# Optimization experiments

Hardware: AMD Instinct MI355X
Metric: run time of the kernel (lower is better)

The kernel has to match this reference:

```python
import jax, jax.numpy as jnp
import numpy as np

F = 128
NRBF = 20
CUTOFF = 5.0
L = 3
NZ = 100
F2 = F // 2
N = 10000
E = 256000
NMOL = 100
EPS = 1e-8


def setup_inputs() -> dict:
    key = jax.random.key(0)
    ks = jax.random.split(key, 20)
    xyz = jax.random.uniform(ks[0], (N, 3), jnp.float32) * 10.0
    z = jax.random.randint(ks[1], (N,), 0, NZ)
    nbrs = jax.random.randint(ks[2], (E, 2), 0, N)
    # avoid self-edges (would give zero distance in the sinc RBF)
    nbrs = nbrs.at[:, 1].set(jnp.where(nbrs[:, 1] == nbrs[:, 0], (nbrs[:, 1] + 1) % N, nbrs[:, 1]))
    mol_idx = jnp.sort(jax.random.randint(ks[3], (N,), 0, NMOL))

    def p(k, shape, scale=0.05):
        return jax.random.normal(k, shape, jnp.float32) * scale

    return dict(
        xyz=xyz, z=z, nbrs=nbrs, mol_idx=mol_idx,
        emb=p(ks[4], (NZ, F), 1.0),
        msg_W1=p(ks[5], (L, F, F)), msg_b1=jnp.zeros((L, F), jnp.float32),
        msg_W2=p(ks[6], (L, F, 3 * F)), msg_b2=jnp.zeros((L, 3 * F), jnp.float32),
        dist_W=p(ks[7], (L, NRBF, 3 * F)), dist_b=jnp.zeros((L, 3 * F), jnp.float32),
        upd_U=p(ks[8], (L, F, F)), upd_V=p(ks[9], (L, F, F)),
        upd_W1=p(ks[10], (L, 2 * F, F)), upd_b1=jnp.zeros((L, F), jnp.float32),
        upd_W2=p(ks[11], (L, F, 3 * F)), upd_b2=jnp.zeros((L, 3 * F), jnp.float32),
        read_W1=p(ks[12], (F, F2)), read_b1=jnp.zeros((F2,), jnp.float32),
        read_W2=p(ks[13], (F2, 1)), read_b2=jnp.zeros((1,), jnp.float32),
    )


def _painn(xyz, emb, msg_W1, msg_b1, msg_W2, msg_b2, dist_W, dist_b,
           upd_U, upd_V, upd_W1, upd_b1, upd_W2, upd_b2,
           read_W1, read_b1, read_W2, read_b2, z, nbrs, mol_idx):
    idx_i = nbrs[:, 0]
    idx_j = nbrs[:, 1]
    r_ij = xyz[idx_j] - xyz[idx_i]                       # [E,3]
    d = jnp.sqrt(jnp.sum(r_ij * r_ij, -1) + EPS)          # [E]
    unit = r_ij / d[:, None]
    # sinc radial basis + cosine cutoff envelope
    nvec = jnp.arange(1, NRBF + 1, dtype=xyz.dtype)
    rbf = jnp.sin(nvec[None, :] * jnp.pi * d[:, None] / CUTOFF) / d[:, None]   # [E,NRBF]
    fcut = 0.5 * (jnp.cos(jnp.pi * d / CUTOFF) + 1.0) * (d < CUTOFF)           # [E]

    s_i = emb[z]                                          # [N,F]
    v_i = jnp.zeros((xyz.shape[0], F, 3), xyz.dtype)      # [N,F,3]

    for l in range(L):
        # message block: invariant filter on nodes, gather to edges
        phi = (jax.nn.silu(s_i @ msg_W1[l] + msg_b1[l]) @ msg_W2[l] + msg_b2[l])[idx_j]  # [E,3F]
        w_s = (rbf @ dist_W[l] + dist_b[l]) * fcut[:, None]                               # [E,3F]
        inv = (phi * w_s).reshape(-1, 3, F)
        ds_edge = inv[:, 0]                                                               # [E,F]
        dv_edge = inv[:, 1][:, :, None] * v_i[idx_j] + inv[:, 2][:, :, None] * unit[:, None, :]  # [E,F,3]
        s_i = s_i + jax.ops.segment_sum(ds_edge, idx_i, num_segments=s_i.shape[0])
        v_i = v_i + jax.ops.segment_sum(dv_edge, idx_i, num_segments=s_i.shape[0])

        # update block: channel-mixing of vectors + gated scalar/vector residuals
        u_v = jnp.einsum('nfv,fg->ngv', v_i, upd_U[l])
        v_v = jnp.einsum('nfv,fg->ngv', v_i, upd_V[l])
        vnorm = jnp.sqrt(jnp.sum(v_v * v_v, -1) + EPS)                                    # [N,F]
        a = (jax.nn.silu(jnp.concatenate([s_i, vnorm], -1) @ upd_W1[l] + upd_b1[l])
             @ upd_W2[l] + upd_b2[l]).reshape(-1, 3, F)
        dv = u_v * a[:, 0][:, :, None]
        ds = a[:, 1] * jnp.sum(u_v * v_v, -1) + a[:, 2]
        s_i = s_i + ds
        v_i = v_i + dv

    atom_e = jax.nn.silu(s_i @ read_W1 + read_b1) @ read_W2 + read_b2                     # [N,1]
    energy = jax.ops.segment_sum(atom_e[:, 0], mol_idx, num_segments=NMOL)                # [NMOL]
    return energy


def reference(xyz, z, nbrs, mol_idx, emb, msg_W1, msg_b1, msg_W2, msg_b2,
              dist_W, dist_b, upd_U, upd_V, upd_W1, upd_b1, upd_W2, upd_b2,
              read_W1, read_b1, read_W2, read_b2):
    return _painn(xyz, emb, msg_W1, msg_b1, msg_W2, msg_b2, dist_W, dist_b,
                  upd_U, upd_V, upd_W1, upd_b1, upd_W2, upd_b2,
                  read_W1, read_b1, read_W2, read_b2, z, nbrs, mol_idx)
```

## Files before the change

### kernel.cpp

```cpp
#include <hip/hip_runtime.h>
#include <hip/hip_bf16.h>
#include <math.h>

#define NA 10000
#define NE 256000
#define FDIM 128
#define F3 384
#define NRBF 20
#define NLAYERS 3
#define NMOLS 100
#define CAP 96
#define WROW 388
#define CUTOFF_F 5.0f
#define EPS_F 1e-8f
#define PI_F 3.14159265358979323846f

typedef __attribute__((ext_vector_type(8))) short bf16x8;
typedef __attribute__((ext_vector_type(4))) short bf16x4;
typedef __attribute__((ext_vector_type(4))) float f32x4;

__device__ __forceinline__ float silu_f(float x) { return x / (1.0f + __expf(-x)); }

__device__ __forceinline__ unsigned short f2bf(float x) {
  unsigned u = __float_as_uint(x);
  return (unsigned short)((u + 0x7FFFu + ((u >> 16) & 1u)) >> 16);
}
__device__ __forceinline__ float bf2f(unsigned short u) {
  return __uint_as_float(((unsigned)u) << 16);
}

__global__ __launch_bounds__(256) void geom_build_kernel(
    const float* __restrict__ xyz, const int* __restrict__ nbrs,
    float* __restrict__ unitv, unsigned short* __restrict__ rbf_bf,
    float* __restrict__ fcut,
    int* __restrict__ deg, int* __restrict__ slot_e, int* __restrict__ slot_j) {
  int e = blockIdx.x * 256 + threadIdx.x;
  if (e >= NE) return;
  int i = nbrs[2 * e + 0], j = nbrs[2 * e + 1];
  float rx = xyz[3 * j + 0] - xyz[3 * i + 0];
  float ry = xyz[3 * j + 1] - xyz[3 * i + 1];
  float rz = xyz[3 * j + 2] - xyz[3 * i + 2];
  float d = sqrtf(rx * rx + ry * ry + rz * rz + EPS_F);
  if (d >= CUTOFF_F) return;
  float invd = 1.0f / d;
  float fc = 0.5f * (__cosf(PI_F * d / CUTOFF_F) + 1.0f);
  unitv[3 * e + 0] = rx * invd;
  unitv[3 * e + 1] = ry * invd;
  unitv[3 * e + 2] = rz * invd;
  fcut[e] = fc;
  float base = PI_F * d / CUTOFF_F;
  float sc = invd * fc;
#pragma unroll
  for (int k = 0; k < NRBF; k++)
    rbf_bf[(size_t)e * NRBF + k] = f2bf(__sinf((float)(k + 1) * base) * sc);
  int pos = atomicAdd(&deg[i], 1);
  if (pos < CAP) {
    slot_e[i * CAP + pos] = e;
    slot_j[i * CAP + pos] = j;
  }
}

__device__ __forceinline__ void pack_one(const float* __restrict__ src,
                                         unsigned short* __restrict__ dst,
                                         int loc, int per, int N) {
  int lay = loc / per;
  int kn = loc - lay * per;
  int k = kn / N, n = kn - k * N;
  int kb = k >> 5, q = (k >> 3) & 3, j = k & 7, nt = n >> 4, c = n & 15;
  int NT = N >> 4;
  dst[(size_t)lay * per + (((kb * NT + nt) * 64 + (q * 16 + c)) * 8 + j)] = f2bf(src[loc]);
}

__device__ __forceinline__ void pack_dw(const float* __restrict__ dW,
                                        const float* __restrict__ db,
                                        unsigned short* __restrict__ dst, int loc) {
  int lay = loc / 12288;
  int kn = loc - lay * 12288;
  int k = kn / 384, n = kn - k * 384;
  float val = 0.0f;
  if (k < NRBF) val = dW[lay * NRBF * 384 + k * 384 + n];
  else if (k == NRBF) val = db[lay * 384 + n];
  int q = (k >> 3) & 3, j = k & 7, nt = n >> 4, c = n & 15;
  dst[(size_t)lay * 12288 + ((nt * 64 + (q * 16 + c)) * 8 + j)] = f2bf(val);
}

__global__ __launch_bounds__(256) void pack_all_kernel(
    const float* __restrict__ msgW1, const float* __restrict__ msgW2,
    const float* __restrict__ updU, const float* __restrict__ updV,
    const float* __restrict__ updW1, const float* __restrict__ updW2,
    const float* __restrict__ rW1, const float* __restrict__ distW,
    const float* __restrict__ distb, unsigned short* __restrict__ dst) {
  int t = blockIdx.x * 256 + threadIdx.x;
  if (t < 49152) pack_one(msgW1, dst, t, 16384, 128);
  else if (t < 196608) pack_one(msgW2, dst + 49152, t - 49152, 49152, 384);
  else if (t < 245760) pack_one(updU, dst + 196608, t - 196608, 16384, 128);
  else if (t < 294912) pack_one(updV, dst + 245760, t - 245760, 16384, 128);
  else if (t < 393216) pack_one(updW1, dst + 294912, t - 294912, 32768, 128);
  else if (t < 540672) pack_one(updW2, dst + 393216, t - 393216, 49152, 384);
  else if (t < 548864) pack_one(rW1, dst + 540672, t - 540672, 8192, 64);
  else if (t < 585728) pack_dw(distW, distb, dst + 548864, t - 548864);
}

__global__ __launch_bounds__(256) void msg0_mfma_kernel(
    const float* __restrict__ emb, const int* __restrict__ z, float* __restrict__ s_out,
    const unsigned short* __restrict__ pW1, const float* __restrict__ b1,
    const unsigned short* __restrict__ pW2, const float* __restrict__ b2,
    bf16x4* __restrict__ phi4) {
  __shared__ bf16x8 sA[4 * 64];
  __shared__ bf16x8 hA[4 * 64];
  int a0 = blockIdx.x * 16;
  int t = threadIdx.x;
  int lane = t & 63, w = t >> 6;
  {
    int kb = t >> 6, l = t & 63;
    int m = l & 15, q = l >> 4;
    int zi = z[a0 + m];
    const float* sp = emb + (size_t)zi * FDIM + kb * 32 + q * 8;
    float* so = s_out + (size_t)(a0 + m) * FDIM + kb * 32 + q * 8;
    bf16x8 c;
#pragma unroll
    for (int j = 0; j < 8; j++) {
      float v = sp[j];
      so[j] = v;
      c[j] = (short)f2bf(v);
    }
    sA[kb * 64 + l] = c;
  }
  __syncthreads();
  f32x4 accH[2];
#pragma unroll
  for (int t2 = 0; t2 < 2; t2++)
#pragma unroll
    for (int r = 0; r < 4; r++) accH[t2][r] = 0.0f;
  const bf16x8* W1f = (const bf16x8*)pW1;
#pragma unroll
  for (int kb = 0; kb < 4; kb++) {
    bf16x8 a = sA[kb * 64 + lane];
#pragma unroll
    for (int t2 = 0; t2 < 2; t2++) {
      bf16x8 b = W1f[(kb * 8 + 2 * w + t2) * 64 + lane];
      accH[t2] = __builtin_amdgcn_mfma_f32_16x16x32_bf16(a, b, accH[t2], 0, 0, 0);
    }
  }
  short* hs = (short*)hA;
#pragma unroll
  for (int t2 = 0; t2 < 2; t2++) {
    int n = w * 32 + t2 * 16 + (lane & 15);
    int kb = n >> 5, q = (n >> 3) & 3, j = n & 7;
    float bias = b1[n];
#pragma unroll
    for (int r = 0; r < 4; r++) {
      int m = (lane >> 4) * 4 + r;
      hs[(kb * 64 + q * 16 + m) * 8 + j] = (short)f2bf(silu_f(accH[t2][r] + bias));
    }
  }
  __syncthreads();
  f32x4 accP[3][2];
#pragma unroll
  for (int c3 = 0; c3 < 3; c3++)
#pragma unroll
    for (int t2 = 0; t2 < 2; t2++)
#pragma unroll
      for (int r = 0; r < 4; r++) accP[c3][t2][r] = 0.0f;
  const bf16x8* W2f = (const bf16x8*)pW2;
#pragma unroll
  for (int kb = 0; kb < 4; kb++) {
    bf16x8 a = hA[kb * 64 + lane];
#pragma unroll
    for (int c3 = 0; c3 < 3; c3++)
#pragma unroll
      for (int t2 = 0; t2 < 2; t2++) {
        bf16x8 b = W2f[(kb * 24 + c3 * 8 + 2 * w + t2) * 64 + lane];
        accP[c3][t2] = __builtin_amdgcn_mfma_f32_16x16x32_bf16(a, b, accP[c3][t2], 0, 0, 0);
      }
  }
#pragma unroll
  for (int t2 = 0; t2 < 2; t2++) {
    int g = (2 * w + t2) * 16 + (lane & 15);
    float bb0 = b2[g], bb1 = b2[FDIM + g], bb2 = b2[2 * FDIM + g];
#pragma unroll
    for (int r = 0; r < 4; r++) {
      int m = (lane >> 4) * 4 + r;
      bf16x4 pw;
      pw[0] = (short)f2bf(accP[0][t2][r] + bb0);
      pw[1] = (short)f2bf(accP[1][t2][r] + bb1);
      pw[2] = (short)f2bf(accP[2][t2][r] + bb2);
      pw[3] = 0;
      phi4[(size_t)(a0 + m) * FDIM + g] = pw;
    }
  }
}

__global__ __launch_bounds__(128) void edge_kernel(
    const bf16x4* __restrict__ phi4, const bf16x4* __restrict__ vpad4,
    unsigned short* __restrict__ v_lin, float* __restrict__ s,
    const unsigned short* __restrict__ pDW,
    const int* __restrict__ deg, const int* __restrict__ slot_e,
    const int* __restrict__ slot_j, const unsigned short* __restrict__ rbf_bf,
    const float* __restrict__ fcut, const float* __restrict__ unitv, int vzero) {
  __shared__ bf16x8 aLDS[64];
  __shared__ unsigned short w_lds[16][WROW];
  __shared__ float l_u[16][3];
  __shared__ int l_j[16];
  int i = blockIdx.x;
  int t = threadIdx.x;
  int f = t;
  int lane = t & 63, w = t >> 6;
  int cnt = deg[i];
  if (cnt > CAP) cnt = CAP;
  int base = i * CAP;
  float acc_s = 0.f, av0 = 0.f, av1 = 0.f, av2 = 0.f;
  const bf16x8* Bf = (const bf16x8*)pDW;
  for (int c0 = 0; c0 < cnt; c0 += 16) {
    int ccnt = cnt - c0;
    if (ccnt > 16) ccnt = 16;
    __syncthreads();
    if (t < 64) {
      int m = t & 15, q = t >> 4;
      bf16x8 a;
#pragma unroll
      for (int j = 0; j < 8; j++) a[j] = 0;
      int p = c0 + m;
      if (p < cnt) {
        int e = slot_e[base + p];
        const unsigned short* rb = rbf_bf + (size_t)e * NRBF;
#pragma unroll
        for (int j = 0; j < 8; j++) {
          int k = q * 8 + j;
          if (k < NRBF) a[j] = (short)rb[k];
          else if (k == NRBF) a[j] = (short)f2bf(fcut[e]);
        }
      }
      aLDS[t] = a;
    } else if (t < 80) {
      int idx = t - 64;
      int p = c0 + idx;
      if (p < cnt) {
        int e = slot_e[base + p];
        l_j[idx] = slot_j[base + p];
        l_u[idx][0] = unitv[3 * e + 0];
        l_u[idx][1] = unitv[3 * e + 1];
        l_u[idx][2] = unitv[3 * e + 2];
      }
    }
    __syncthreads();
    {
      bf16x8 a = aLDS[lane];
      int n0 = lane & 15, m0 = (lane >> 4) * 4;
#pragma unroll
      for (int tt = 0; tt < 12; tt++) {
        int nt = 12 * w + tt;
        f32x4 acc;
#pragma unroll
        for (int r = 0; r < 4; r++) acc[r] = 0.0f;
        acc = __builtin_amdgcn_mfma_f32_16x16x32_bf16(a, Bf[nt * 64 + lane], acc, 0, 0, 0);
        int n = nt * 16 + n0;
#pragma unroll
        for (int r = 0; r < 4; r++) w_lds[m0 + r][n] = f2bf(acc[r]);
      }
    }
    __syncthreads();
    int pp = 0;
    for (; pp + 2 <= ccnt; pp += 2) {
      int j0 = l_j[pp], j1 = l_j[pp + 1];
      bf16x4 P0 = phi4[(size_t)j0 * FDIM + f];
      bf16x4 P1 = phi4[(size_t)j1 * FDIM + f];
      float v00 = 0.f, v01 = 0.f, v02 = 0.f, v10 = 0.f, v11 = 0.f, v12 = 0.f;
      if (!vzero) {
        bf16x4 V0 = vpad4[(size_t)j0 * FDIM + f];
        bf16x4 V1 = vpad4[(size_t)j1 * FDIM + f];
        v00 = bf2f((unsigned short)V0[0]); v01 = bf2f((unsigned short)V0[1]); v02 = bf2f((unsigned short)V0[2]);
        v10 = bf2f((unsigned short)V1[0]); v11 = bf2f((unsigned short)V1[1]); v12 = bf2f((unsigned short)V1[2]);
      }
      float p00 = bf2f((unsigned short)P0[0]), p01 = bf2f((unsigned short)P0[1]), p02 = bf2f((unsigned short)P0[2]);
      float p10 = bf2f((unsigned short)P1[0]), p11 = bf2f((unsigned short)P1[1]), p12 = bf2f((unsigned short)P1[2]);
      float w00 = bf2f(w_lds[pp][f]), w01 = bf2f(w_lds[pp][FDIM + f]),
            w02 = bf2f(w_lds[pp][2 * FDIM + f]);
      float w10 = bf2f(w_lds[pp + 1][f]), w11 = bf2f(w_lds[pp + 1][FDIM + f]),
            w12 = bf2f(w_lds[pp + 1][2 * FDIM + f]);
      acc_s += p00 * w00 + p10 * w10;
      float i01 = p01 * w01, i02 = p02 * w02, i11 = p11 * w11, i12 = p12 * w12;
      av0 += i01 * v00 + i02 * l_u[pp][0] + i11 * v10 + i12 * l_u[pp + 1][0];
      av1 += i01 * v01 + i02 * l_u[pp][1] + i11 * v11 + i12 * l_u[pp + 1][1];
      av2 += i01 * v02 + i02 * l_u[pp][2] + i11 * v12 + i12 * l_u[pp + 1][2];
    }
    if (pp < ccnt) {
      int j0 = l_j[pp];
      bf16x4 P0 = phi4[(size_t)j0 * FDIM + f];
      float v00 = 0.f, v01 = 0.f, v02 = 0.f;
      if (!vzero) {
        bf16x4 V0 = vpad4[(size_t)j0 * FDIM + f];
        v00 = bf2f((unsigned short)V0[0]); v01 = bf2f((unsigned short)V0[1]); v02 = bf2f((unsigned short)V0[2]);
      }
      float p00 = bf2f((unsigned short)P0[0]), p01 = bf2f((unsigned short)P0[1]), p02 = bf2f((unsigned short)P0[2]);
      float w00 = bf2f(w_lds[pp][f]), w01 = bf2f(w_lds[pp][FDIM + f]),
            w02 = bf2f(w_lds[pp][2 * FDIM + f]);
      acc_s += p00 * w00;
      float i01 = p01 * w01, i02 = p02 * w02;
      av0 += i01 * v00 + i02 * l_u[pp][0];
      av1 += i01 * v01 + i02 * l_u[pp][1];
      av2 += i01 * v02 + i02 * l_u[pp][2];
    }
  }
  if (!vzero) {
    bf16x4 VI = vpad4[(size_t)i * FDIM + f];
    av0 += bf2f((unsigned short)VI[0]);
    av1 += bf2f((unsigned short)VI[1]);
    av2 += bf2f((unsigned short)VI[2]);
  }
  unsigned short* vlo = v_lin + (size_t)i * F3;
  vlo[f] = f2bf(av0);
  vlo[FDIM + f] = f2bf(av1);
  vlo[2 * FDIM + f] = f2bf(av2);
  s[(size_t)i * FDIM + f] += acc_s;
}

__global__ __launch_bounds__(256) void upd_fused_kernel(
    float* __restrict__ s, const unsigned short* __restrict__ v_lin,
    bf16x4* __restrict__ vpad4,
    const unsigned short* __restrict__ pU, const unsigned short* __restrict__ pV,
    const unsigned short* __restrict__ pW1, const float* __restrict__ b1,
    const unsigned short* __restrict__ pW2, const float* __restrict__ b2,
    int mode,
    const unsigned short* __restrict__ pMW1, const float* __restrict__ mb1,
    const unsigned short* __restrict__ pMW2, const float* __restrict__ mb2,
    bf16x4* __restrict__ phi4,
    const unsigned short* __restrict__ pRW1, const float* __restrict__ rb1,
    const float* __restrict__ rW2, const float* __restrict__ rb2,
    float* __restrict__ atom_e) {
  __shared__ bf16x8 vAf[3 * 4 * 64];
  __shared__ bf16x8 catA[8 * 64];
  __shared__ bf16x8 hA[4 * 64];
  __shared__ float red[4][16];
  int a0 = blockIdx.x * 16;
  int t = threadIdx.x;
  int lane = t & 63, w = t >> 6;
  {
    int l = t & 63, kb = (t >> 6) & 3;
    int m = l & 15, q = l >> 4;
#pragma unroll
    for (int rt = 0; rt < 3; rt++) {
      vAf[(rt * 4 + kb) * 64 + l] =
          *(const bf16x8*)(v_lin + (size_t)(a0 + m) * F3 + rt * FDIM + kb * 32 + q * 8);
    }
    const float* sp = s + (size_t)(a0 + m) * FDIM + kb * 32 + q * 8;
    bf16x8 c;
#pragma unroll
    for (int j = 0; j < 8; j++) c[j] = (short)f2bf(sp[j]);
    catA[kb * 64 + l] = c;
  }
  __syncthreads();
  f32x4 accU[3][2], accV[3][2];
#pragma unroll
  for (int rt = 0; rt < 3; rt++)
#pragma unroll
    for (int t2 = 0; t2 < 2; t2++)
#pragma unroll
      for (int r = 0; r < 4; r++) { accU[rt][t2][r] = 0.0f; accV[rt][t2][r] = 0.0f; }
  const bf16x8* Uf = (const bf16x8*)pU;
  const bf16x8* Vf = (const bf16x8*)pV;
#pragma unroll
  for (int kb = 0; kb < 4; kb++) {
    bf16x8 bu[2], bv[2];
#pragma unroll
    for (int t2 = 0; t2 < 2; t2++) {
      bu[t2] = Uf[(kb * 8 + 2 * w + t2) * 64 + lane];
      bv[t2] = Vf[(kb * 8 + 2 * w + t2) * 64 + lane];
    }
#pragma unroll
    for (int rt = 0; rt < 3; rt++) {
      bf16x8 a = vAf[(rt * 4 + kb) * 64 + lane];
#pragma unroll
      for (int t2 = 0; t2 < 2; t2++) {
        accU[rt][t2] = __builtin_amdgcn_mfma_f32_16x16x32_bf16(a, bu[t2], accU[rt][t2], 0, 0, 0);
        accV[rt][t2] = __builtin_amdgcn_mfma_f32_16x16x32_bf16(a, bv[t2], accV[rt][t2], 0, 0, 0);
      }
    }
  }
  short* cs = (short*)catA;
#pragma unroll
  for (int t2 = 0; t2 < 2; t2++) {
    int g = w * 32 + t2 * 16 + (lane & 15);
    int k = 128 + g;
    int kb = k >> 5, q = (k >> 3) & 3, j = k & 7;
#pragma unroll
    for (int r = 0; r < 4; r++) {
      int m = (lane >> 4) * 4 + r;
      float x0 = accV[0][t2][r], x1 = accV[1][t2][r], x2 = accV[2][t2][r];
      cs[(kb * 64 + q * 16 + m) * 8 + j] = (short)f2bf(sqrtf(x0 * x0 + x1 * x1 + x2 * x2 + EPS_F));
    }
  }
  __syncthreads();
  f32x4 accH[2];
#pragma unroll
  for (int t2 = 0; t2 < 2; t2++)
#pragma unroll
    for (int r = 0; r < 4; r++) accH[t2][r] = 0.0f;
  const bf16x8* W1f = (const bf16x8*)pW1;
#pragma unroll
  for (int kb = 0; kb < 8; kb++) {
    bf16x8 a = catA[kb * 64 + lane];
#pragma unroll
    for (int t2 = 0; t2 < 2; t2++) {
      bf16x8 b = W1f[(kb * 8 + 2 * w + t2) * 64 + lane];
      accH[t2] = __builtin_amdgcn_mfma_f32_16x16x32_bf16(a, b, accH[t2], 0, 0, 0);
    }
  }
  short* hs = (short*)hA;
#pragma unroll
  for (int t2 = 0; t2 < 2; t2++) {
    int n = w * 32 + t2 * 16 + (lane & 15);
    int kb = n >> 5, q = (n >> 3) & 3, j = n & 7;
    float bias = b1[n];
#pragma unroll
    for (int r = 0; r < 4; r++) {
      int m = (lane >> 4) * 4 + r;
      hs[(kb * 64 + q * 16 + m) * 8 + j] = (short)f2bf(silu_f(accH[t2][r] + bias));
    }
  }
  __syncthreads();
  f32x4 accA[3][2];
#pragma unroll
  for (int c3 = 0; c3 < 3; c3++)
#pragma unroll
    for (int t2 = 0; t2 < 2; t2++)
#pragma unroll
      for (int r = 0; r < 4; r++) accA[c3][t2][r] = 0.0f;
  const bf16x8* W2f = (const bf16x8*)pW2;
#pragma unroll
  for (int kb = 0; kb < 4; kb++) {
    bf16x8 a = hA[kb * 64 + lane];
#pragma unroll
    for (int c3 = 0; c3 < 3; c3++)
#pragma unroll
      for (int t2 = 0; t2 < 2; t2++) {
        bf16x8 b = W2f[(kb * 24 + c3 * 8 + 2 * w + t2) * 64 + lane];
        accA[c3][t2] = __builtin_amdgcn_mfma_f32_16x16x32_bf16(a, b, accA[c3][t2], 0, 0, 0);
      }
  }
#pragma unroll
  for (int t2 = 0; t2 < 2; t2++) {
    int g = w * 32 + t2 * 16 + (lane & 15);
    float bb0 = b2[g], bb1 = b2[FDIM + g], bb2 = b2[2 * FDIM + g];
    int kb = g >> 5, q = (g >> 3) & 3, j = g & 7;
#pragma unroll
    for (int r = 0; r < 4; r++) {
      int m = (lane >> 4) * 4 + r;
      int n = a0 + m;
      float a0v = accA[0][t2][r] + bb0;
      float a1v = accA[1][t2][r] + bb1;
      float a2v = accA[2][t2][r] + bb2;
      float dot = accU[0][t2][r] * accV[0][t2][r] + accU[1][t2][r] * accV[1][t2][r] +
                  accU[2][t2][r] * accV[2][t2][r];
      float s_new = s[(size_t)n * FDIM + g] + a1v * dot + a2v;
      if (mode == 0) {
        s[(size_t)n * FDIM + g] = s_new;
        bf16x4 vw;
#pragma unroll
        for (int c = 0; c < 3; c++) {
          float nv = bf2f(v_lin[(size_t)n * F3 + c * FDIM + g]) + a0v * accU[c][t2][r];
          vw[c] = (short)f2bf(nv);
        }
        vw[3] = 0;
        vpad4[(size_t)n * FDIM + g] = vw;
      }
      cs[(kb * 64 + q * 16 + m) * 8 + j] = (short)f2bf(s_new);
    }
  }
  __syncthreads();
  if (mode == 0) {
    f32x4 accH2[2];
#pragma unroll
    for (int t2 = 0; t2 < 2; t2++)
#pragma unroll
      for (int r = 0; r < 4; r++) accH2[t2][r] = 0.0f;
    const bf16x8* MW1f = (const bf16x8*)pMW1;
#pragma unroll
    for (int kb = 0; kb < 4; kb++) {
      bf16x8 a = catA[kb * 64 + lane];
#pragma unroll
      for (int t2 = 0; t2 < 2; t2++) {
        bf16x8 b = MW1f[(kb * 8 + 2 * w + t2) * 64 + lane];
        accH2[t2] = __builtin_amdgcn_mfma_f32_16x16x32_bf16(a, b, accH2[t2], 0, 0, 0);
      }
    }
#pragma unroll
    for (int t2 = 0; t2 < 2; t2++) {
      int n = w * 32 + t2 * 16 + (lane & 15);
      int kb = n >> 5, q = (n >> 3) & 3, j = n & 7;
      float bias = mb1[n];
#pragma unroll
      for (int r = 0; r < 4; r++) {
        int m = (lane >> 4) * 4 + r;
        hs[(kb * 64 + q * 16 + m) * 8 + j] = (short)f2bf(silu_f(accH2[t2][r] + bias));
      }
    }
    __syncthreads();
    f32x4 accP[3][2];
#pragma unroll
    for (int c3 = 0; c3 < 3; c3++)
#pragma unroll
      for (int t2 = 0; t2 < 2; t2++)
#pragma unroll
        for (int r = 0; r < 4; r++) accP[c3][t2][r] = 0.0f;
    const bf16x8* MW2f = (const bf16x8*)pMW2;
#pragma unroll
    for (int kb = 0; kb < 4; kb++) {
      bf16x8 a = hA[kb * 64 + lane];
#pragma unroll
      for (int c3 = 0; c3 < 3; c3++)
#pragma unroll
        for (int t2 = 0; t2 < 2; t2++) {
          bf16x8 b = MW2f[(kb * 24 + c3 * 8 + 2 * w + t2) * 64 + lane];
          accP[c3][t2] = __builtin_amdgcn_mfma_f32_16x16x32_bf16(a, b, accP[c3][t2], 0, 0, 0);
        }
    }
#pragma unroll
    for (int t2 = 0; t2 < 2; t2++) {
      int g = (2 * w + t2) * 16 + (lane & 15);
      float bb0 = mb2[g], bb1 = mb2[FDIM + g], bb2v = mb2[2 * FDIM + g];
#pragma unroll
      for (int r = 0; r < 4; r++) {
        int m = (lane >> 4) * 4 + r;
        bf16x4 pw;
        pw[0] = (short)f2bf(accP[0][t2][r] + bb0);
        pw[1] = (short)f2bf(accP[1][t2][r] + bb1);
        pw[2] = (short)f2bf(accP[2][t2][r] + bb2v);
        pw[3] = 0;
        phi4[(size_t)(a0 + m) * FDIM + g] = pw;
      }
    }
  } else {
    f32x4 acc;
#pragma unroll
    for (int r = 0; r < 4; r++) acc[r] = 0.0f;
    const bf16x8* RW1f = (const bf16x8*)pRW1;
#pragma unroll
    for (int kb = 0; kb < 4; kb++) {
      bf16x8 a = catA[kb * 64 + lane];
      bf16x8 b = RW1f[(kb * 4 + w) * 64 + lane];
      acc = __builtin_amdgcn_mfma_f32_16x16x32_bf16(a, b, acc, 0, 0, 0);
    }
    int col = w * 16 + (lane & 15);
    float bias = rb1[col], w2v = rW2[col];
    float val[4];
#pragma unroll
    for (int r = 0; r < 4; r++) val[r] = silu_f(acc[r] + bias) * w2v;
#pragma unroll
    for (int off = 1; off < 16; off <<= 1)
#pragma unroll
      for (int r = 0; r < 4; r++) val[r] += __shfl_xor(val[r], off, 64);
    if ((lane & 15) == 0) {
#pragma unroll
      for (int r = 0; r < 4; r++) red[w][(lane >> 4) * 4 + r] = val[r];
    }
    __syncthreads();
    if (t < 16) {
      atom_e[a0 + t] = red[0][t] + red[1][t] + red[2][t] + red[3][t] + rb2[0];
    }
  }
}

__global__ __launch_bounds__(256) void mol_reduce_kernel(
    const float* __restrict__ atom_e, const int* __restrict__ mol_idx,
    float* __restrict__ out) {
  __shared__ float molsum[NMOLS];
  int t = threadIdx.x;
  if (t < NMOLS) molsum[t] = 0.0f;
  __syncthreads();
  int n = blockIdx.x * 256 + t;
  if (n < NA) atomicAdd(&molsum[mol_idx[n]], atom_e[n]);
  __syncthreads();
  if (t < NMOLS && molsum[t] != 0.0f) atomicAdd(&out[t], molsum[t]);
}

extern "C" void kernel_launch(void* const* d_in, const int* in_sizes, int n_in,
                              void* d_out, int out_size, void* d_ws, size_t ws_size,
                              hipStream_t stream) {
  const float* xyz = (const float*)d_in[0];
  const int* z = (const int*)d_in[1];
  const int* nbrs = (const int*)d_in[2];
  const int* mol = (const int*)d_in[3];
  const float* emb = (const float*)d_in[4];
  const float* msgW1 = (const float*)d_in[5];
  const float* msgb1 = (const float*)d_in[6];
  const float* msgW2 = (const float*)d_in[7];
  const float* msgb2 = (const float*)d_in[8];
  const float* distW = (const float*)d_in[9];
  const float* distb = (const float*)d_in[10];
  const float* updU = (const float*)d_in[11];
  const float* updV = (const float*)d_in[12];
  const float* updW1 = (const float*)d_in[13];
  const float* updb1 = (const float*)d_in[14];
  const float* updW2 = (const float*)d_in[15];
  const float* updb2 = (const float*)d_in[16];
  const float* rW1 = (const float*)d_in[17];
  const float* rb1 = (const float*)d_in[18];
  const float* rW2 = (const float*)d_in[19];
  const float* rb2 = (const float*)d_in[20];

  float* ws = (float*)d_ws;
  float* s = ws;      ws += (size_t)NA * FDIM;
  float* fcut = ws;   ws += (size_t)NE;
  float* unitv = ws;  ws += (size_t)NE * 3;
  float* atom_e = ws; ws += (size_t)NA;
  int* deg = (int*)ws;
  int* slot_e = deg + NA;
  int* slot_j = slot_e + NA * CAP;
  unsigned short* pk = (unsigned short*)(((uintptr_t)(slot_j + NA * CAP) + 15) & ~(uintptr_t)15);
  unsigned short* pMsgW1 = pk;
  unsigned short* pMsgW2 = pMsgW1 + 49152;
  unsigned short* pUpdU  = pMsgW2 + 147456;
  unsigned short* pUpdV  = pUpdU + 49152;
  unsigned short* pUpdW1 = pUpdV + 49152;
  unsigned short* pUpdW2 = pUpdW1 + 98304;
  unsigned short* pRW1   = pUpdW2 + 147456;
  unsigned short* pDW    = pRW1 + 8192;
  unsigned short* rbf_bf = (unsigned short*)(((uintptr_t)(pDW + 36864) + 15) & ~(uintptr_t)15);
  unsigned short* after_rbf = rbf_bf + (size_t)NE * NRBF + 8;
  bf16x4* phi4 = (bf16x4*)(((uintptr_t)after_rbf + 15) & ~(uintptr_t)15);
  bf16x4* vpad4 = phi4 + (size_t)NA * FDIM;
  unsigned short* v_lin = (unsigned short*)(vpad4 + (size_t)NA * FDIM);

  hipMemsetAsync(deg, 0, NA * sizeof(int), stream);
  hipMemsetAsync(d_out, 0, NMOLS * sizeof(float), stream);

  pack_all_kernel<<<(585728 + 255) / 256, 256, 0, stream>>>(
      msgW1, msgW2, updU, updV, updW1, updW2, rW1, distW, distb, pMsgW1);
  geom_build_kernel<<<NE / 256, 256, 0, stream>>>(xyz, nbrs, unitv, rbf_bf, fcut,
                                                  deg, slot_e, slot_j);
  msg0_mfma_kernel<<<NA / 16, 256, 0, stream>>>(emb, z, s, pMsgW1, msgb1, pMsgW2, msgb2, phi4);

  for (int l = 0; l < NLAYERS; l++) {
    edge_kernel<<<NA, 128, 0, stream>>>(phi4, vpad4, v_lin, s,
                                        pDW + (size_t)l * 12288,
                                        deg, slot_e, slot_j, rbf_bf, fcut, unitv,
                                        (l == 0) ? 1 : 0);
    int mode = (l == NLAYERS - 1) ? 1 : 0;
    int lnext = (l + 1 < NLAYERS) ? l + 1 : 0;
    upd_fused_kernel<<<NA / 16, 256, 0, stream>>>(
        s, v_lin, vpad4, pUpdU + (size_t)l * 16384, pUpdV + (size_t)l * 16384,
        pUpdW1 + (size_t)l * 32768, updb1 + (size_t)l * FDIM,
        pUpdW2 + (size_t)l * 49152, updb2 + (size_t)l * F3,
        mode,
        pMsgW1 + (size_t)lnext * 16384, msgb1 + (size_t)lnext * FDIM,
        pMsgW2 + (size_t)lnext * 49152, msgb2 + (size_t)lnext * F3,
        phi4, pRW1, rb1, rW2, rb2, atom_e);
  }
  mol_reduce_kernel<<<(NA + 255) / 256, 256, 0, stream>>>(atom_e, mol, (float*)d_out);
}
```

Before: 337.7 us.

## Interleave phi and vector features into one packed 12-byte record per atom-feature

The separate padded phi and v gather arrays are merged into a single 6-bf16 record per atom and feature. The edge kernel now issues one 12-byte gather per neighbour instead of two 8-byte gathers, which cuts gathered bytes and memory requests in the later layers. The update kernel stages the new v values in shared memory so they can be written alongside the next layer's phi. The trade-off is that layer 0 now loads the zero-filled v fields it previously skipped, and reusing the shared-memory buffer adds an aliasing risk.

After: 326.4 us. 1.03x faster.

```diff
diff --git a/kernel.cpp b/kernel.cpp
--- a/kernel.cpp
+++ b/kernel.cpp
@@ -16,8 +16,9 @@
 #define PI_F 3.14159265358979323846f
 
 typedef __attribute__((ext_vector_type(8))) short bf16x8;
-typedef __attribute__((ext_vector_type(4))) short bf16x4;
 typedef __attribute__((ext_vector_type(4))) float f32x4;
+
+struct pv6 { unsigned int u0, u1, u2; };
 
 __device__ __forceinline__ float silu_f(float x) { return x / (1.0f + __expf(-x)); }
 
@@ -28,6 +29,8 @@
 __device__ __forceinline__ float bf2f(unsigned short u) {
   return __uint_as_float(((unsigned)u) << 16);
 }
+__device__ __forceinline__ float lo_f(unsigned int u) { return bf2f((unsigned short)(u & 0xFFFFu)); }
+__device__ __forceinline__ float hi_f(unsigned int u) { return bf2f((unsigned short)(u >> 16)); }
 
 __global__ __launch_bounds__(256) void geom_build_kernel(
     const float* __restrict__ xyz, const int* __restrict__ nbrs,
@@ -105,7 +108,7 @@
     const float* __restrict__ emb, const int* __restrict__ z, float* __restrict__ s_out,
     const unsigned short* __restrict__ pW1, const float* __restrict__ b1,
     const unsigned short* __restrict__ pW2, const float* __restrict__ b2,
-    bf16x4* __restrict__ phi4) {
+    pv6* __restrict__ cmb) {
   __shared__ bf16x8 sA[4 * 64];
   __shared__ bf16x8 hA[4 * 64];
   int a0 = blockIdx.x * 16;
@@ -181,23 +184,24 @@
 #pragma unroll
     for (int r = 0; r < 4; r++) {
       int m = (lane >> 4) * 4 + r;
-      bf16x4 pw;
-      pw[0] = (short)f2bf(accP[0][t2][r] + bb0);
-      pw[1] = (short)f2bf(accP[1][t2][r] + bb1);
-      pw[2] = (short)f2bf(accP[2][t2][r] + bb2);
-      pw[3] = 0;
-      phi4[(size_t)(a0 + m) * FDIM + g] = pw;
+      unsigned p0 = f2bf(accP[0][t2][r] + bb0);
+      unsigned p1 = f2bf(accP[1][t2][r] + bb1);
+      unsigned p2 = f2bf(accP[2][t2][r] + bb2);
+      pv6 rec;
+      rec.u0 = p0 | (p1 << 16);
+      rec.u1 = p2;
+      rec.u2 = 0;
+      cmb[(size_t)(a0 + m) * FDIM + g] = rec;
     }
   }
 }
 
 __global__ __launch_bounds__(128) void edge_kernel(
-    const bf16x4* __restrict__ phi4, const bf16x4* __restrict__ vpad4,
-    unsigned short* __restrict__ v_lin, float* __restrict__ s,
-    const unsigned short* __restrict__ pDW,
+    const pv6* __restrict__ cmb, unsigned short* __restrict__ v_lin,
+    float* __restrict__ s, const unsigned short* __restrict__ pDW,
     const int* __restrict__ deg, const int* __restrict__ slot_e,
     const int* __restrict__ slot_j, const unsigned short* __restrict__ rbf_bf,
-    const float* __restrict__ fcut, const float* __restrict__ unitv, int vzero) {
+    const float* __restrict__ fcut, const float* __restrict__ unitv) {
   __shared__ bf16x8 aLDS[64];
   __shared__ unsigned short w_lds[16][WROW];
   __shared__ float l_u[16][3];
@@ -263,17 +267,12 @@
     int pp = 0;
     for (; pp + 2 <= ccnt; pp += 2) {
       int j0 = l_j[pp], j1 = l_j[pp + 1];
-      bf16x4 P0 = phi4[(size_t)j0 * FDIM + f];
-      bf16x4 P1 = phi4[(size_t)j1 * FDIM + f];
-      float v00 = 0.f, v01 = 0.f, v02 = 0.f, v10 = 0.f, v11 = 0.f, v12 = 0.f;
-      if (!vzero) {
-        bf16x4 V0 = vpad4[(size_t)j0 * FDIM + f];
-        bf16x4 V1 = vpad4[(size_t)j1 * FDIM + f];
-        v00 = bf2f((unsigned short)V0[0]); v01 = bf2f((unsigned short)V0[1]); v02 = bf2f((unsigned short)V0[2]);
-        v10 = bf2f((unsigned short)V1[0]); v11 = bf2f((unsigned short)V1[1]); v12 = bf2f((unsigned short)V1[2]);
-      }
-      float p00 = bf2f((unsigned short)P0[0]), p01 = bf2f((unsigned short)P0[1]), p02 = bf2f((unsigned short)P0[2]);
-      float p10 = bf2f((unsigned short)P1[0]), p11 = bf2f((unsigned short)P1[1]), p12 = bf2f((unsigned short)P1[2]);
+      pv6 R0 = cmb[(size_t)j0 * FDIM + f];
+      pv6 R1 = cmb[(size_t)j1 * FDIM + f];
+      float p00 = lo_f(R0.u0), p01 = hi_f(R0.u0), p02 = lo_f(R0.u1);
+      float v00 = hi_f(R0.u1), v01 = lo_f(R0.u2), v02 = hi_f(R0.u2);
+      float p10 = lo_f(R1.u0), p11 = hi_f(R1.u0), p12 = lo_f(R1.u1);
+      float v10 = hi_f(R1.u1), v11 = lo_f(R1.u2), v12 = hi_f(R1.u2);
       float w00 = bf2f(w_lds[pp][f]), w01 = bf2f(w_lds[pp][FDIM + f]),
             w02 = bf2f(w_lds[pp][2 * FDIM + f]);
       float w10 = bf2f(w_lds[pp + 1][f]), w11 = bf2f(w_lds[pp + 1][FDIM + f]),
@@ -286,13 +285,9 @@
     }
     if (pp < ccnt) {
       int j0 = l_j[pp];
-      bf16x4 P0 = phi4[(size_t)j0 * FDIM + f];
-      float v00 = 0.f, v01 = 0.f, v02 = 0.f;
-      if (!vzero) {
-        bf16x4 V0 = vpad4[(size_t)j0 * FDIM + f];
-        v00 = bf2f((unsigned short)V0[0]); v01 = bf2f((unsigned short)V0[1]); v02 = bf2f((unsigned short)V0[2]);
-      }
-      float p00 = bf2f((unsigned short)P0[0]), p01 = bf2f((unsigned short)P0[1]), p02 = bf2f((unsigned short)P0[2]);
+      pv6 R0 = cmb[(size_t)j0 * FDIM + f];
+      float p00 = lo_f(R0.u0), p01 = hi_f(R0.u0), p02 = lo_f(R0.u1);
+      float v00 = hi_f(R0.u1), v01 = lo_f(R0.u2), v02 = hi_f(R0.u2);
       float w00 = bf2f(w_lds[pp][f]), w01 = bf2f(w_lds[pp][FDIM + f]),
             w02 = bf2f(w_lds[pp][2 * FDIM + f]);
       acc_s += p00 * w00;
@@ -302,11 +297,11 @@
       av2 += i01 * v02 + i02 * l_u[pp][2];
     }
   }
-  if (!vzero) {
-    bf16x4 VI = vpad4[(size_t)i * FDIM + f];
-    av0 += bf2f((unsigned short)VI[0]);
-    av1 += bf2f((unsigned short)VI[1]);
-    av2 += bf2f((unsigned short)VI[2]);
+  {
+    pv6 RI = cmb[(size_t)i * FDIM + f];
+    av0 += hi_f(RI.u1);
+    av1 += lo_f(RI.u2);
+    av2 += hi_f(RI.u2);
   }
   unsigned short* vlo = v_lin + (size_t)i * F3;
   vlo[f] = f2bf(av0);
@@ -317,14 +312,13 @@
 
 __global__ __launch_bounds__(256) void upd_fused_kernel(
     float* __restrict__ s, const unsigned short* __restrict__ v_lin,
-    bf16x4* __restrict__ vpad4,
+    pv6* __restrict__ cmb,
     const unsigned short* __restrict__ pU, const unsigned short* __restrict__ pV,
     const unsigned short* __restrict__ pW1, const float* __restrict__ b1,
     const unsigned short* __restrict__ pW2, const float* __restrict__ b2,
     int mode,
     const unsigned short* __restrict__ pMW1, const float* __restrict__ mb1,
     const unsigned short* __restrict__ pMW2, const float* __restrict__ mb2,
-    bf16x4* __restrict__ phi4,
     const unsigned short* __restrict__ pRW1, const float* __restrict__ rb1,
     const float* __restrict__ rW2, const float* __restrict__ rb2,
     float* __restrict__ atom_e) {
@@ -438,6 +432,7 @@
         accA[c3][t2] = __builtin_amdgcn_mfma_f32_16x16x32_bf16(a, b, accA[c3][t2], 0, 0, 0);
       }
   }
+  short* vsc = (short*)vAf;
 #pragma unroll
   for (int t2 = 0; t2 < 2; t2++) {
     int g = w * 32 + t2 * 16 + (lane & 15);
@@ -455,14 +450,11 @@
       float s_new = s[(size_t)n * FDIM + g] + a1v * dot + a2v;
       if (mode == 0) {
         s[(size_t)n * FDIM + g] = s_new;
-        bf16x4 vw;
 #pragma unroll
         for (int c = 0; c < 3; c++) {
           float nv = bf2f(v_lin[(size_t)n * F3 + c * FDIM + g]) + a0v * accU[c][t2][r];
-          vw[c] = (short)f2bf(nv);
+          vsc[(m * FDIM + g) * 3 + c] = (short)f2bf(nv);
         }
-        vw[3] = 0;
-        vpad4[(size_t)n * FDIM + g] = vw;
       }
       cs[(kb * 64 + q * 16 + m) * 8 + j] = (short)f2bf(s_new);
     }
@@ -522,12 +514,17 @@
 #pragma unroll
       for (int r = 0; r < 4; r++) {
         int m = (lane >> 4) * 4 + r;
-        bf16x4 pw;
-        pw[0] = (short)f2bf(accP[0][t2][r] + bb0);
-        pw[1] = (short)f2bf(accP[1][t2][r] + bb1);
-        pw[2] = (short)f2bf(accP[2][t2][r] + bb2v);
-        pw[3] = 0;
-        phi4[(size_t)(a0 + m) * FDIM + g] = pw;
+        unsigned p0 = f2bf(accP[0][t2][r] + bb0);
+        unsigned p1 = f2bf(accP[1][t2][r] + bb1);
+        unsigned p2 = f2bf(accP[2][t2][r] + bb2v);
+        unsigned v0 = (unsigned short)vsc[(m * FDIM + g) * 3 + 0];
+        unsigned v1 = (unsigned short)vsc[(m * FDIM + g) * 3 + 1];
+        unsigned v2 = (unsigned short)vsc[(m * FDIM + g) * 3 + 2];
+        pv6 rec;
+        rec.u0 = p0 | (p1 << 16);
+        rec.u1 = p2 | (v0 << 16);
+        rec.u2 = v1 | (v2 << 16);
+        cmb[(size_t)(a0 + m) * FDIM + g] = rec;
       }
     }
   } else {
@@ -618,9 +615,8 @@
   unsigned short* pDW    = pRW1 + 8192;
   unsigned short* rbf_bf = (unsigned short*)(((uintptr_t)(pDW + 36864) + 15) & ~(uintptr_t)15);
   unsigned short* after_rbf = rbf_bf + (size_t)NE * NRBF + 8;
-  bf16x4* phi4 = (bf16x4*)(((uintptr_t)after_rbf + 15) & ~(uintptr_t)15);
-  bf16x4* vpad4 = phi4 + (size_t)NA * FDIM;
-  unsigned short* v_lin = (unsigned short*)(vpad4 + (size_t)NA * FDIM);
+  pv6* cmb = (pv6*)(((uintptr_t)after_rbf + 15) & ~(uintptr_t)15);
+  unsigned short* v_lin = (unsigned short*)(cmb + (size_t)NA * FDIM);
 
   hipMemsetAsync(deg, 0, NA * sizeof(int), stream);
   hipMemsetAsync(d_out, 0, NMOLS * sizeof(float), stream);
@@ -629,23 +625,22 @@
       msgW1, msgW2, updU, updV, updW1, updW2, rW1, distW, distb, pMsgW1);
   geom_build_kernel<<<NE / 256, 256, 0, stream>>>(xyz, nbrs, unitv, rbf_bf, fcut,
                                                   deg, slot_e, slot_j);
-  msg0_mfma_kernel<<<NA / 16, 256, 0, stream>>>(emb, z, s, pMsgW1, msgb1, pMsgW2, msgb2, phi4);
+  msg0_mfma_kernel<<<NA / 16, 256, 0, stream>>>(emb, z, s, pMsgW1, msgb1, pMsgW2, msgb2, cmb);
 
   for (int l = 0; l < NLAYERS; l++) {
-    edge_kernel<<<NA, 128, 0, stream>>>(phi4, vpad4, v_lin, s,
+    edge_kernel<<<NA, 128, 0, stream>>>(cmb, v_lin, s,
                                         pDW + (size_t)l * 12288,
-                                        deg, slot_e, slot_j, rbf_bf, fcut, unitv,
-                                        (l == 0) ? 1 : 0);
+                                        deg, slot_e, slot_j, rbf_bf, fcut, unitv);
     int mode = (l == NLAYERS - 1) ? 1 : 0;
     int lnext = (l + 1 < NLAYERS) ? l + 1 : 0;
     upd_fused_kernel<<<NA / 16, 256, 0, stream>>>(
-        s, v_lin, vpad4, pUpdU + (size_t)l * 16384, pUpdV + (size_t)l * 16384,
+        s, v_lin, cmb, pUpdU + (size_t)l * 16384, pUpdV + (size_t)l * 16384,
         pUpdW1 + (size_t)l * 32768, updb1 + (size_t)l * FDIM,
         pUpdW2 + (size_t)l * 49152, updb2 + (size_t)l * F3,
         mode,
         pMsgW1 + (size_t)lnext * 16384, msgb1 + (size_t)lnext * FDIM,
         pMsgW2 + (size_t)lnext * 49152, msgb2 + (size_t)lnext * F3,
-        phi4, pRW1, rb1, rW2, rb2, atom_e);
+        pRW1, rb1, rW2, rb2, atom_e);
   }
   mol_reduce_kernel<<<(NA + 255) / 256, 256, 0, stream>>>(atom_e, mol, (float*)d_out);
 }
```
